# Kernel tuning notes

Hardware: AMD Instinct MI355X
Metric: run time of the kernel (lower is better)

Reference implementation:

```python
import jax, jax.numpy as jnp
import numpy as np

S = 512          # data_patch_size -> grid of S x S vertices
BS = 16          # batch size
EPS = 1e-12      # torch F.normalize eps


def _make_faces(h, w):
    # standard grid triangulation: each quad -> two triangles
    idx = np.arange(h * w).reshape(h, w)
    v00 = idx[:-1, :-1].ravel(); v01 = idx[:-1, 1:].ravel()
    v10 = idx[1:, :-1].ravel();  v11 = idx[1:, 1:].ravel()
    t1 = np.stack([v00, v10, v01], axis=1)
    t2 = np.stack([v01, v10, v11], axis=1)
    return np.concatenate([t1, t2], axis=0).astype(np.int64)


def _vertex_tri_maps(faces, n_verts):
    # vectorized version of VertexNormals.vertex_tri_maps:
    # per-vertex list of incident face ids, zero-padded, weights = 1/deg (0 on pad)
    fv = faces.ravel()
    fid = np.repeat(np.arange(faces.shape[0], dtype=np.int64), 3)
    order = np.argsort(fv, kind='stable')
    fv_s, fid_s = fv[order], fid[order]
    counts = np.bincount(fv, minlength=n_verts)
    starts = np.concatenate([[0], np.cumsum(counts)[:-1]])
    pos = np.arange(fv_s.size) - starts[fv_s]
    c = int(counts.max())  # == 6 for a grid mesh
    vti = np.zeros((n_verts, c), dtype=np.int64)
    vti[fv_s, pos] = fid_s
    col = np.arange(c)[None, :]
    w = np.where(col < counts[:, None], 1.0 / np.maximum(counts, 1)[:, None], 0.0)
    return vti, w.astype(np.float32)[None, :, :, None]  # [1, r, c, 1]


def setup_inputs() -> dict:
    key = jax.random.key(0)
    n_verts = S * S
    faces = _make_faces(S, S)                        # [F, 3]
    vti, vtw = _vertex_tri_maps(faces, n_verts)      # [r, c], [1, r, c, 1]
    vrt = jax.random.normal(key, (BS, n_verts, 3), dtype=jnp.float32)
    return {
        'vrt': vrt,
        'faces': jnp.asarray(faces),
        'vert_tri_indices': jnp.asarray(vti),
        'vert_tri_weights': jnp.asarray(vtw),
    }


def _normalize(x):
    # torch F.normalize(p=2): x / max(||x||, eps)
    n = jnp.sqrt(jnp.sum(x * x, axis=-1, keepdims=True))
    return x / jnp.maximum(n, EPS)


def reference(vrt, faces, vert_tri_indices, vert_tri_weights):
    # face normals: cross of two edge vectors, normalized
    p0 = vrt[:, faces[:, 0]]                         # [bs, F, 3]
    v1 = vrt[:, faces[:, 1]] - p0
    v2 = vrt[:, faces[:, 2]] - p0
    face_normals = _normalize(jnp.cross(v1, v2))     # [bs, F, 3]
    # gather incident face normals per vertex, weighted sum, normalize
    fn_group = face_normals[:, vert_tri_indices]     # [bs, r, c, 3]
    vertex_normals = jnp.sum(fn_group * vert_tri_weights, axis=-2)  # [bs, r, 3]
    return _normalize(vertex_normals)
```

## Files before the change

kernel.cpp:

```cpp
#include <hip/hip_runtime.h>

#define SS 512
#define NVERT (SS * SS)
#define NBATCH 16

struct V3 { float x, y, z; };

__device__ __forceinline__ V3 loadv(const float* __restrict__ p, int idx) {
    const float* q = p + 3 * (size_t)idx;
    V3 r; r.x = q[0]; r.y = q[1]; r.z = q[2]; return r;
}

__device__ __forceinline__ V3 subv(V3 a, V3 b) { return {a.x - b.x, a.y - b.y, a.z - b.z}; }

__device__ __forceinline__ V3 crossv(V3 a, V3 b) {
    return {a.y * b.z - a.z * b.y,
            a.z * b.x - a.x * b.z,
            a.x * b.y - a.y * b.x};
}

__device__ __forceinline__ float rsq_eps(float d) {
    return __builtin_amdgcn_rsqf(fmaxf(d, 1e-24f));
}

__global__ __launch_bounds__(256) void VertexNormals_kernel(
        const float* __restrict__ vrt, float* __restrict__ out) {
    int tid = blockIdx.x * blockDim.x + threadIdx.x;
    int b = tid >> 18;
    int v = tid & (NVERT - 1);
    int r = v >> 9;
    int c = v & (SS - 1);

    const float* base = vrt + (size_t)b * (3 * NVERT);

    int rm1 = (r > 0)      ? r - 1 : 0;
    int rp1 = (r < SS - 1) ? r + 1 : SS - 1;
    int cm1 = (c > 0)      ? c - 1 : 0;
    int cp1 = (c < SS - 1) ? c + 1 : SS - 1;

    V3 pcc = loadv(base, r   * SS + c  );
    V3 pmc = loadv(base, rm1 * SS + c  );
    V3 ppc = loadv(base, rp1 * SS + c  );
    V3 pcm = loadv(base, r   * SS + cm1);
    V3 pcp = loadv(base, r   * SS + cp1);
    V3 pmp = loadv(base, rm1 * SS + cp1);
    V3 ppm = loadv(base, rp1 * SS + cm1);

    bool rm = (r > 0), rp = (r < SS - 1), cm = (c > 0), cp = (c < SS - 1);

    float ax = 0.f, ay = 0.f, az = 0.f;
    auto addf = [&](V3 p0, V3 p1, V3 p2) {
        V3 u = subv(p1, p0);
        V3 w = subv(p2, p0);
        V3 n = crossv(u, w);
        float inv = rsq_eps(n.x * n.x + n.y * n.y + n.z * n.z);
        ax += n.x * inv; ay += n.y * inv; az += n.z * inv;
    };

    if (rp & cp) addf(pcc, ppc, pcp);
    if (rm & cp) { addf(pmc, pcc, pmp); addf(pmp, pcc, pcp); }
    if (rp & cm) { addf(pcm, ppm, pcc); addf(pcc, ppm, ppc); }
    if (rm & cm) addf(pmc, pcm, pcc);

    float inv = rsq_eps(ax * ax + ay * ay + az * az);

    float* o = out + 3 * (size_t)tid;
    o[0] = ax * inv; o[1] = ay * inv; o[2] = az * inv;
}

extern "C" void kernel_launch(void* const* d_in, const int* in_sizes, int n_in,
                              void* d_out, int out_size, void* d_ws, size_t ws_size,
                              hipStream_t stream) {
    const float* vrt = (const float*)d_in[0];
    float* out = (float*)d_out;

    const int total = NBATCH * NVERT;
    const int block = 256;
    const int grid = total / block;

    hipLaunchKernelGGL(VertexNormals_kernel, dim3(grid), dim3(block), 0, stream,
                       vrt, out);
}
```

Before: 124.3 us.

## Process four vertices per thread with float4 row loads and block swizzle

Each thread now computes four consecutive vertices of one row. It loads 3 rows of neighbours with vectorized float4 loads and writes results as three float4 stores, which removes the scalar strided 12-byte accesses. A block index swizzle spreads consecutive blocks across batches and rows, probably for better cache or channel locality. This adds register pressure, and there is some redundant recomputation of face normals between neighbouring vertices.

```diff
diff --git a/kernel.cpp b/kernel.cpp
--- a/kernel.cpp
+++ b/kernel.cpp
@@ -2,70 +2,97 @@
 
 #define SS 512
 #define NVERT (SS * SS)
+#define ROWF (SS * 3)
 #define NBATCH 16
 
 struct V3 { float x, y, z; };
-
-__device__ __forceinline__ V3 loadv(const float* __restrict__ p, int idx) {
-    const float* q = p + 3 * (size_t)idx;
-    V3 r; r.x = q[0]; r.y = q[1]; r.z = q[2]; return r;
-}
-
-__device__ __forceinline__ V3 subv(V3 a, V3 b) { return {a.x - b.x, a.y - b.y, a.z - b.z}; }
-
-__device__ __forceinline__ V3 crossv(V3 a, V3 b) {
-    return {a.y * b.z - a.z * b.y,
-            a.z * b.x - a.x * b.z,
-            a.x * b.y - a.y * b.x};
-}
 
 __device__ __forceinline__ float rsq_eps(float d) {
     return __builtin_amdgcn_rsqf(fmaxf(d, 1e-24f));
 }
 
+__device__ __forceinline__ void addf(V3& acc, V3 p0, V3 p1, V3 p2) {
+    float ux = p1.x - p0.x, uy = p1.y - p0.y, uz = p1.z - p0.z;
+    float wx = p2.x - p0.x, wy = p2.y - p0.y, wz = p2.z - p0.z;
+    float nx = uy * wz - uz * wy;
+    float ny = uz * wx - ux * wz;
+    float nz = ux * wy - uy * wx;
+    float inv = rsq_eps(nx * nx + ny * ny + nz * nz);
+    acc.x += nx * inv; acc.y += ny * inv; acc.z += nz * inv;
+}
+
+__device__ __forceinline__ void load_row(const float* __restrict__ rowp, int t, V3 (&p)[6]) {
+    if (t == 0) {
+        const float4* w = reinterpret_cast<const float4*>(rowp);
+        float4 a0 = w[0], a1 = w[1], a2 = w[2], a3 = w[3];
+        p[1] = {a0.x, a0.y, a0.z};
+        p[0] = p[1];
+        p[2] = {a0.w, a1.x, a1.y};
+        p[3] = {a1.z, a1.w, a2.x};
+        p[4] = {a2.y, a2.z, a2.w};
+        p[5] = {a3.x, a3.y, a3.z};
+    } else {
+        const float4* w = reinterpret_cast<const float4*>(rowp + 12 * t - 4);
+        float4 a0 = w[0], a1 = w[1], a2 = w[2], a3 = w[3];
+        p[0] = {a0.y, a0.z, a0.w};
+        p[1] = {a1.x, a1.y, a1.z};
+        p[2] = {a1.w, a2.x, a2.y};
+        p[3] = {a2.z, a2.w, a3.x};
+        p[4] = {a3.y, a3.z, a3.w};
+        if (t < 127) {
+            float4 a4 = w[4];
+            p[5] = {a4.x, a4.y, a4.z};
+        } else {
+            p[5] = p[4];
+        }
+    }
+}
+
 __global__ __launch_bounds__(256) void VertexNormals_kernel(
         const float* __restrict__ vrt, float* __restrict__ out) {
-    int tid = blockIdx.x * blockDim.x + threadIdx.x;
-    int b = tid >> 18;
-    int v = tid & (NVERT - 1);
-    int r = v >> 9;
-    int c = v & (SS - 1);
+    int bid = blockIdx.x;
+    int swz = ((bid & 7) << 9) | (bid >> 3);
+    int tid = threadIdx.x;
+    int t = tid & 127;
+    int b = swz >> 8;
+    int r = ((swz & 255) << 1) | (tid >> 7);
 
     const float* base = vrt + (size_t)b * (3 * NVERT);
+    int rm1 = (r > 0) ? r - 1 : 0;
+    int rp1 = (r < SS - 1) ? r + 1 : SS - 1;
 
-    int rm1 = (r > 0)      ? r - 1 : 0;
-    int rp1 = (r < SS - 1) ? r + 1 : SS - 1;
-    int cm1 = (c > 0)      ? c - 1 : 0;
-    int cp1 = (c < SS - 1) ? c + 1 : SS - 1;
+    V3 A[6], B[6], C[6];
+    load_row(base + (size_t)rm1 * ROWF, t, A);
+    load_row(base + (size_t)r   * ROWF, t, B);
+    load_row(base + (size_t)rp1 * ROWF, t, C);
 
-    V3 pcc = loadv(base, r   * SS + c  );
-    V3 pmc = loadv(base, rm1 * SS + c  );
-    V3 ppc = loadv(base, rp1 * SS + c  );
-    V3 pcm = loadv(base, r   * SS + cm1);
-    V3 pcp = loadv(base, r   * SS + cp1);
-    V3 pmp = loadv(base, rm1 * SS + cp1);
-    V3 ppm = loadv(base, rp1 * SS + cm1);
+    bool rm = (r > 0), rp = (r < SS - 1);
 
-    bool rm = (r > 0), rp = (r < SS - 1), cm = (c > 0), cp = (c < SS - 1);
+    float res[12];
+    #pragma unroll
+    for (int i = 0; i < 4; ++i) {
+        bool cm = (t > 0) || (i > 0);
+        bool cp = (t < 127) || (i < 3);
+        V3 pcm = B[i],     pcc = B[i + 1], pcp = B[i + 2];
+        V3 pmc = A[i + 1], pmp = A[i + 2];
+        V3 ppm = C[i],     ppc = C[i + 1];
 
-    float ax = 0.f, ay = 0.f, az = 0.f;
-    auto addf = [&](V3 p0, V3 p1, V3 p2) {
-        V3 u = subv(p1, p0);
-        V3 w = subv(p2, p0);
-        V3 n = crossv(u, w);
-        float inv = rsq_eps(n.x * n.x + n.y * n.y + n.z * n.z);
-        ax += n.x * inv; ay += n.y * inv; az += n.z * inv;
-    };
+        V3 acc = {0.f, 0.f, 0.f};
+        if (rp && cp) addf(acc, pcc, ppc, pcp);
+        if (rm && cp) { addf(acc, pmc, pcc, pmp); addf(acc, pmp, pcc, pcp); }
+        if (rp && cm) { addf(acc, pcm, ppm, pcc); addf(acc, pcc, ppm, ppc); }
+        if (rm && cm) addf(acc, pmc, pcm, pcc);
 
-    if (rp & cp) addf(pcc, ppc, pcp);
-    if (rm & cp) { addf(pmc, pcc, pmp); addf(pmp, pcc, pcp); }
-    if (rp & cm) { addf(pcm, ppm, pcc); addf(pcc, ppm, ppc); }
-    if (rm & cm) addf(pmc, pcm, pcc);
+        float inv = rsq_eps(acc.x * acc.x + acc.y * acc.y + acc.z * acc.z);
+        res[3 * i + 0] = acc.x * inv;
+        res[3 * i + 1] = acc.y * inv;
+        res[3 * i + 2] = acc.z * inv;
+    }
 
-    float inv = rsq_eps(ax * ax + ay * ay + az * az);
-
-    float* o = out + 3 * (size_t)tid;
-    o[0] = ax * inv; o[1] = ay * inv; o[2] = az * inv;
+    float* o = out + ((size_t)b * NVERT + (size_t)r * SS + 4 * (size_t)t) * 3;
+    reinterpret_cast<float4*>(o)[0] = {res[0], res[1], res[2],  res[3]};
+    reinterpret_cast<float4*>(o)[1] = {res[4], res[5], res[6],  res[7]};
+    reinterpret_cast<float4*>(o)[2] = {res[8], res[9], res[10], res[11]};
 }
 
 extern "C" void kernel_launch(void* const* d_in, const int* in_sizes, int n_in,
@@ -74,10 +101,7 @@
     const float* vrt = (const float*)d_in[0];
     float* out = (float*)d_out;
 
-    const int total = NBATCH * NVERT;
-    const int block = 256;
-    const int grid = total / block;
-
-    hipLaunchKernelGGL(VertexNormals_kernel, dim3(grid), dim3(block), 0, stream,
+    const int grid = (NBATCH * SS) / 2;
+    hipLaunchKernelGGL(VertexNormals_kernel, dim3(grid), dim3(256), 0, stream,
                        vrt, out);
 }
```

After: 130.1 us. +4.7%, slower.
